# Kernel tuning notes

Hardware: AMD Instinct MI355X
Metric: run time of the kernel (lower is better)

## Reference

```python
import jax, jax.numpy as jnp
import numpy as np

N = 50000          # num nodes
E = 1_600_000      # num edges (avg degree 32)
F = 512            # node_dim
C = 64             # num_clusters
O = 256            # output_dim


def setup_inputs() -> dict:
    key = jax.random.key(0)
    ks = jax.random.split(key, 9)
    lim_p = 1.0 / np.sqrt(F)
    inp = {
        "x": jax.random.normal(ks[0], (N, F), dtype=jnp.float32),
        "edge_index": jax.random.randint(ks[1], (2, E), 0, N, dtype=jnp.int64),
        "batch": jnp.zeros((N,), dtype=jnp.int64),
        # gnn_pool: Linear(F, C)
        "Wp": jax.random.uniform(ks[2], (F, C), jnp.float32, -lim_p, lim_p),
        "bp": jax.random.uniform(ks[3], (C,), jnp.float32, -lim_p, lim_p),
        # gnn_embed: Linear(F, F)
        "We": jax.random.uniform(ks[4], (F, F), jnp.float32, -lim_p, lim_p),
        "be": jax.random.uniform(ks[5], (F,), jnp.float32, -lim_p, lim_p),
        # projection: Linear(F, O)
        "Wo": jax.random.uniform(ks[6], (F, O), jnp.float32, -lim_p, lim_p),
        "bo": jax.random.uniform(ks[7], (O,), jnp.float32, -lim_p, lim_p),
    }
    return inp


def reference(x, edge_index, batch, Wp, bp, We, be, Wo, bo):
    # s = softmax(gnn_pool(x), -1): soft cluster assignments  [N, C]
    s = jax.nn.softmax(x @ Wp + bp, axis=-1)
    # h = gnn_embed(x)  [N, F]
    h = x @ We + be
    # dense_diff_pool pooled features: out = s^T h  -> [C, F]
    # (out_adj = s^T A s and the link/entropy reg are computed by the
    #  original but discarded; they do not affect the returned output.)
    pooled = jnp.einsum("nc,nf->cf", s, h)
    # PyG dense_diff_pool unsqueezes 2D inputs to batch dim 1 -> [1, C, F]
    out = pooled[None] @ Wo + bo  # [1, C, O]
    return out
```

## Files before the change

kernel.cpp:

```cpp
#include <hip/hip_runtime.h>
#include <hip/hip_bf16.h>

typedef __attribute__((ext_vector_type(8))) short short8;
typedef __attribute__((ext_vector_type(4))) float floatx4;
typedef __attribute__((ext_vector_type(4))) unsigned uint4v;

#define FDIM 512
#define CDIM 64
#define ODIM 256
#define TR   32
#define XSF  516
#define STS 40
#define MAXP 512
#define RSW(r) ((((r) >> 3) & 3) << 2)

__device__ __forceinline__ ushort f2bf(float f) {
    union { float f; unsigned u; } v; v.f = f;
    unsigned r = v.u + 0x7FFFu + ((v.u >> 16) & 1u);
    return (ushort)(r >> 16);
}
__device__ __forceinline__ float bf2f(unsigned hi16) {
    union { unsigned u; float f; } v; v.u = hi16 << 16; return v.f;
}

__device__ __forceinline__ void gld16(const float* g, float* lds_base) {
    __builtin_amdgcn_global_load_lds(
        (const __attribute__((address_space(1))) unsigned int*)(const void*)g,
        (__attribute__((address_space(3))) unsigned int*)(void*)lds_base,
        16, 0, 0);
}

__global__ __launch_bounds__(256) void kWpT(const float* __restrict__ Wp,
                                            ushort* __restrict__ WpT) {
    int g = blockIdx.x * 256 + threadIdx.x;
    int f = g >> 6, c = g & 63;
    WpT[c * FDIM + f] = f2bf(Wp[f * CDIM + c]);
}

__global__ __launch_bounds__(512, 2) void kFused(
        const float* __restrict__ x, const ushort* __restrict__ WpT,
        const float* __restrict__ bp, ushort* __restrict__ part,
        float* __restrict__ cpart, int N, int nTiles, int P) {
    __shared__ float  xsf[TR * XSF + 16];
    __shared__ ushort sT[CDIM][STS];
    __shared__ float  red1[TR][4];
    __shared__ float  red2[TR][4];
    __shared__ float  cred[CDIM][2];

    const int t    = threadIdx.x;
    const int w    = t >> 6;
    const int lane = t & 63;
    const int l16  = lane & 15;
    const int q    = lane >> 4;
    const int ci   = w & 3;
    const int rg   = w >> 2;

    floatx4 acc[4][4];
#pragma unroll
    for (int mt = 0; mt < 4; ++mt)
#pragma unroll
        for (int nt = 0; nt < 4; ++nt) acc[mt][nt] = (floatx4){0.f, 0.f, 0.f, 0.f};
    float csp[4] = {0.f, 0.f, 0.f, 0.f};

    float bpv[4];
#pragma unroll
    for (int reg = 0; reg < 4; ++reg) bpv[reg] = bp[16 * ci + 4 * q + reg];

    const ushort* wb = WpT + (size_t)(16 * ci + l16) * FDIM + q * 8;

    for (int tile = blockIdx.x; tile < nTiles; tile += P) {
        __syncthreads();
        const int row0 = tile * TR;

#pragma unroll
        for (int i = 0; i < 8; ++i) {
            const int c0 = w * 8 + i;
            const int r  = c0 >> 1;
            const int h  = c0 & 1;
            float* lb = xsf + r * XSF + RSW(r) + h * 256;
            if (row0 + r < N) {
                const float* g = x + (size_t)(row0 + r) * FDIM + h * 256 + lane * 4;
                gld16(g, lb);
            } else {
                *(floatx4*)(lb + lane * 4) = (floatx4){0.f, 0.f, 0.f, 0.f};
            }
        }
        __syncthreads();

        floatx4 acc1 = (floatx4){0.f, 0.f, 0.f, 0.f};
        const int prow = 16 * rg + l16;
        const float* xr = xsf + prow * XSF + RSW(prow);
#pragma unroll
        for (int kb = 0; kb < 4; ++kb) {
            short8 af[4];
#pragma unroll
            for (int ki = 0; ki < 4; ++ki)
                af[ki] = *(const short8*)(wb + kb * 128 + ki * 32);
#pragma unroll
            for (int ki = 0; ki < 4; ++ki) {
                const int off = kb * 128 + ki * 32 + q * 8;
                floatx4 u0 = *(const floatx4*)(xr + off);
                floatx4 u1 = *(const floatx4*)(xr + off + 4);
                short8 b;
                b[0] = (short)f2bf(u0[0]); b[1] = (short)f2bf(u0[1]);
                b[2] = (short)f2bf(u0[2]); b[3] = (short)f2bf(u0[3]);
                b[4] = (short)f2bf(u1[0]); b[5] = (short)f2bf(u1[1]);
                b[6] = (short)f2bf(u1[2]); b[7] = (short)f2bf(u1[3]);
                acc1 = __builtin_amdgcn_mfma_f32_16x16x32_bf16(af[ki], b, acc1, 0, 0, 0);
            }
        }

        const int row = prow;
        float lg[4];
#pragma unroll
        for (int reg = 0; reg < 4; ++reg) lg[reg] = acc1[reg] + bpv[reg];
        float m = fmaxf(fmaxf(lg[0], lg[1]), fmaxf(lg[2], lg[3]));
        m = fmaxf(m, __shfl_xor(m, 16));
        m = fmaxf(m, __shfl_xor(m, 32));
        if (lane < 16) red1[16 * rg + lane][ci] = m;
        __syncthreads();
        const float rmax = fmaxf(fmaxf(red1[row][0], red1[row][1]),
                                 fmaxf(red1[row][2], red1[row][3]));
        float p = 0.f;
#pragma unroll
        for (int reg = 0; reg < 4; ++reg) {
            float e = __expf(lg[reg] - rmax);
            lg[reg] = e; p += e;
        }
        p += __shfl_xor(p, 16);
        p += __shfl_xor(p, 32);
        if (lane < 16) red2[16 * rg + lane][ci] = p;
        __syncthreads();
        const float rsi = 1.0f / (red2[row][0] + red2[row][1] +
                                  red2[row][2] + red2[row][3]);
        const bool valid = (row0 + row) < N;
#pragma unroll
        for (int reg = 0; reg < 4; ++reg) {
            float s = valid ? lg[reg] * rsi : 0.f;
            sT[16 * ci + 4 * q + reg][row] = f2bf(s);
            csp[reg] += s;
        }
        __syncthreads();

        short8 as_[4];
#pragma unroll
        for (int mt = 0; mt < 4; ++mt)
            as_[mt] = *(const short8*)&sT[16 * mt + l16][q * 8];
#pragma unroll
        for (int nt = 0; nt < 4; ++nt) {
            const int f = 64 * w + 16 * nt + l16;
            short8 b;
#pragma unroll
            for (int j = 0; j < 8; ++j)
                b[j] = (short)f2bf(xsf[(q * 8 + j) * XSF + 4 * q + f]);
#pragma unroll
            for (int mt = 0; mt < 4; ++mt)
                acc[mt][nt] = __builtin_amdgcn_mfma_f32_16x16x32_bf16(
                    as_[mt], b, acc[mt][nt], 0, 0, 0);
        }
    }

#pragma unroll
    for (int reg = 0; reg < 4; ++reg) {
        float v = csp[reg];
        v += __shfl_xor(v, 1); v += __shfl_xor(v, 2);
        v += __shfl_xor(v, 4); v += __shfl_xor(v, 8);
        if (l16 == 0) cred[16 * ci + 4 * q + reg][rg] = v;
    }
    __syncthreads();
    if (t < 64) cpart[(size_t)blockIdx.x * CDIM + t] = cred[t][0] + cred[t][1];

    ushort* xf = (ushort*)xsf;
#pragma unroll
    for (int mt = 0; mt < 4; ++mt)
#pragma unroll
        for (int nt = 0; nt < 4; ++nt)
#pragma unroll
            for (int reg = 0; reg < 4; ++reg)
                xf[(16 * mt + 4 * q + reg) * FDIM + 64 * w + 16 * nt + l16] =
                    f2bf(acc[mt][nt][reg]);
    __syncthreads();
    const uint4v* src = (const uint4v*)xf;
    uint4v* dst = (uint4v*)(part + (size_t)blockIdx.x * (CDIM * FDIM));
#pragma unroll
    for (int i = 0; i < 8; ++i)
        dst[i * 512 + t] = src[i * 512 + t];
}

__global__ __launch_bounds__(512) void kR(const ushort* __restrict__ part,
                                          const float* __restrict__ cpart,
                                          float* __restrict__ colsum,
                                          float* __restrict__ Mp,
                                          int P, int pch) {
    __shared__ float ws8[8];
    const int c = blockIdx.x, pc = blockIdx.y, t = threadIdx.x;
    const int p0 = pc * pch, p1 = min(p0 + pch, P);

    float sum = 0.f;
    const ushort* pp = part + (size_t)c * FDIM + t;
#pragma unroll 4
    for (int p = p0; p < p1; ++p)
        sum += bf2f((unsigned)pp[(size_t)p * (CDIM * FDIM)]);
    Mp[((size_t)pc * CDIM + c) * FDIM + t] = sum;

    float cv = 0.f;
    {
        int p = p0 + t;
        if (p < p1) cv = cpart[(size_t)p * CDIM + c];
    }
    cv += __shfl_xor(cv, 1);  cv += __shfl_xor(cv, 2);
    cv += __shfl_xor(cv, 4);  cv += __shfl_xor(cv, 8);
    cv += __shfl_xor(cv, 16); cv += __shfl_xor(cv, 32);
    if ((t & 63) == 0) ws8[t >> 6] = cv;
    __syncthreads();
    if (t == 0) {
        float tot = 0.f;
#pragma unroll
        for (int i = 0; i < 8; ++i) tot += ws8[i];
        atomicAdd(colsum + c, tot);
    }
}

__global__ __launch_bounds__(512) void kC(const float* __restrict__ Mp,
                                          const float* __restrict__ colsum,
                                          const float* __restrict__ We,
                                          const float* __restrict__ be,
                                          const float* __restrict__ Wo,
                                          const float* __restrict__ bo,
                                          float* __restrict__ out) {
    __shared__ float Mrow[512];
    __shared__ float pooled[512];
    __shared__ float halves[2][256];
    const int c = blockIdx.x, t = threadIdx.x;

    float sum = 0.f;
#pragma unroll
    for (int pc = 0; pc < 8; ++pc)
        sum += Mp[((size_t)pc * CDIM + c) * FDIM + t];
    Mrow[t] = sum;
    __syncthreads();

    float a = colsum[c] * be[t];
#pragma unroll 16
    for (int k = 0; k < FDIM; ++k)
        a = fmaf(Mrow[k], We[(size_t)k * FDIM + t], a);
    pooled[t] = a;
    __syncthreads();

    const int o = t & 255, h = t >> 8;
    float b = 0.f;
#pragma unroll 16
    for (int kk = 0; kk < 256; ++kk) {
        int k = h * 256 + kk;
        b = fmaf(pooled[k], Wo[(size_t)k * ODIM + o], b);
    }
    halves[h][o] = b;
    __syncthreads();
    if (t < 256)
        out[(size_t)c * ODIM + t] = halves[0][t] + halves[1][t] + bo[t];
}

extern "C" void kernel_launch(void* const* d_in, const int* in_sizes, int n_in,
                              void* d_out, int out_size, void* d_ws, size_t ws_size,
                              hipStream_t stream) {
    const float* x  = (const float*)d_in[0];
    const float* Wp = (const float*)d_in[3];
    const float* bp = (const float*)d_in[4];
    const float* We = (const float*)d_in[5];
    const float* be = (const float*)d_in[6];
    const float* Wo = (const float*)d_in[7];
    const float* bo = (const float*)d_in[8];
    float* out = (float*)d_out;

    const int N = in_sizes[0] / FDIM;
    const int nTiles = (N + TR - 1) / TR;

    char*   wsb    = (char*)d_ws;
    ushort* WpT    = (ushort*)wsb;
    float*  colsum = (float*)(wsb + 65536);
    float*  cpart  = (float*)(wsb + 66560);
    float*  Mp     = (float*)(wsb + 266752);
    const size_t PART_OFF = 1315328;
    ushort* part   = (ushort*)(wsb + PART_OFF);

    size_t avail = (ws_size > PART_OFF + 65536) ? (ws_size - PART_OFF) / 65536 : 1;
    int P = (int)(avail < (size_t)MAXP ? avail : (size_t)MAXP);
    if (P > nTiles) P = nTiles;
    if (P < 1) P = 1;
    const int pch = (P + 7) / 8;

    hipMemsetAsync(colsum, 0, 256, stream);
    kWpT<<<128, 256, 0, stream>>>(Wp, WpT);
    kFused<<<P, 512, 0, stream>>>(x, WpT, bp, part, cpart, N, nTiles, P);
    kR<<<dim3(CDIM, 8), 512, 0, stream>>>(part, cpart, colsum, Mp, P, pch);
    kC<<<CDIM, 512, 0, stream>>>(Mp, colsum, We, be, Wo, bo, out);
}
```

Baseline: 239.5 us.

## Double-buffer x tiles in fused kernel, hoist Wp fragments, vectorize partial reduction

The fused kernel now stages the next x tile into a second LDS buffer while computing on the current one, so global loads overlap the MFMA work. The Wp bf16 fragments are loaded into registers once instead of on every tile. The partial-reduction kernel reads four bf16 values per thread across four interleaved partition groups, which produces 32 partial rows that the final kernel sums. MAXP is halved to 256 to fit the doubled LDS use, and the workspace offsets are enlarged for the bigger Mp buffer. The cost is more registers and LDS per block, which may lower occupancy.

```diff
diff --git a/kernel.cpp b/kernel.cpp
--- a/kernel.cpp
+++ b/kernel.cpp
@@ -4,6 +4,7 @@
 typedef __attribute__((ext_vector_type(8))) short short8;
 typedef __attribute__((ext_vector_type(4))) float floatx4;
 typedef __attribute__((ext_vector_type(4))) unsigned uint4v;
+typedef __attribute__((ext_vector_type(4))) unsigned short ushort4v;
 
 #define FDIM 512
 #define CDIM 64
@@ -11,7 +12,7 @@
 #define TR   32
 #define XSF  516
 #define STS 40
-#define MAXP 512
+#define MAXP 256
 #define RSW(r) ((((r) >> 3) & 3) << 2)
 
 __device__ __forceinline__ ushort f2bf(float f) {
@@ -41,7 +42,7 @@
         const float* __restrict__ x, const ushort* __restrict__ WpT,
         const float* __restrict__ bp, ushort* __restrict__ part,
         float* __restrict__ cpart, int N, int nTiles, int P) {
-    __shared__ float  xsf[TR * XSF + 16];
+    __shared__ float  xsf[2][TR * XSF + 16];
     __shared__ ushort sT[CDIM][STS];
     __shared__ float  red1[TR][4];
     __shared__ float  red2[TR][4];
@@ -67,35 +68,45 @@
     for (int reg = 0; reg < 4; ++reg) bpv[reg] = bp[16 * ci + 4 * q + reg];
 
     const ushort* wb = WpT + (size_t)(16 * ci + l16) * FDIM + q * 8;
-
-    for (int tile = blockIdx.x; tile < nTiles; tile += P) {
-        __syncthreads();
-        const int row0 = tile * TR;
-
+    short8 af[4][4];
+#pragma unroll
+    for (int kb = 0; kb < 4; ++kb)
+#pragma unroll
+        for (int ki = 0; ki < 4; ++ki)
+            af[kb][ki] = *(const short8*)(wb + kb * 128 + ki * 32);
+
+    auto stage = [&](int tile, float* xb) {
+        const int row0s = tile * TR;
 #pragma unroll
         for (int i = 0; i < 8; ++i) {
             const int c0 = w * 8 + i;
             const int r  = c0 >> 1;
             const int h  = c0 & 1;
-            float* lb = xsf + r * XSF + RSW(r) + h * 256;
-            if (row0 + r < N) {
-                const float* g = x + (size_t)(row0 + r) * FDIM + h * 256 + lane * 4;
+            float* lb = xb + r * XSF + RSW(r) + h * 256;
+            if (row0s + r < N) {
+                const float* g = x + (size_t)(row0s + r) * FDIM + h * 256 + lane * 4;
                 gld16(g, lb);
             } else {
                 *(floatx4*)(lb + lane * 4) = (floatx4){0.f, 0.f, 0.f, 0.f};
             }
         }
-        __syncthreads();
+    };
+
+    stage(blockIdx.x, xsf[0]);
+    __syncthreads();
+
+    int it = 0;
+    for (int tile = blockIdx.x; tile < nTiles; tile += P, ++it) {
+        float* xb = xsf[it & 1];
+        if (tile + P < nTiles) stage(tile + P, xsf[(it & 1) ^ 1]);
+
+        const int row0 = tile * TR;
 
         floatx4 acc1 = (floatx4){0.f, 0.f, 0.f, 0.f};
         const int prow = 16 * rg + l16;
-        const float* xr = xsf + prow * XSF + RSW(prow);
+        const float* xr = xb + prow * XSF + RSW(prow);
 #pragma unroll
         for (int kb = 0; kb < 4; ++kb) {
-            short8 af[4];
-#pragma unroll
-            for (int ki = 0; ki < 4; ++ki)
-                af[ki] = *(const short8*)(wb + kb * 128 + ki * 32);
 #pragma unroll
             for (int ki = 0; ki < 4; ++ki) {
                 const int off = kb * 128 + ki * 32 + q * 8;
@@ -106,7 +117,7 @@
                 b[2] = (short)f2bf(u0[2]); b[3] = (short)f2bf(u0[3]);
                 b[4] = (short)f2bf(u1[0]); b[5] = (short)f2bf(u1[1]);
                 b[6] = (short)f2bf(u1[2]); b[7] = (short)f2bf(u1[3]);
-                acc1 = __builtin_amdgcn_mfma_f32_16x16x32_bf16(af[ki], b, acc1, 0, 0, 0);
+                acc1 = __builtin_amdgcn_mfma_f32_16x16x32_bf16(af[kb][ki], b, acc1, 0, 0, 0);
             }
         }
 
@@ -152,12 +163,14 @@
             short8 b;
 #pragma unroll
             for (int j = 0; j < 8; ++j)
-                b[j] = (short)f2bf(xsf[(q * 8 + j) * XSF + 4 * q + f]);
+                b[j] = (short)f2bf(xb[(q * 8 + j) * XSF + 4 * q + f]);
 #pragma unroll
             for (int mt = 0; mt < 4; ++mt)
                 acc[mt][nt] = __builtin_amdgcn_mfma_f32_16x16x32_bf16(
                     as_[mt], b, acc[mt][nt], 0, 0, 0);
         }
+
+        __syncthreads();
     }
 
 #pragma unroll
@@ -194,14 +207,19 @@
                                           int P, int pch) {
     __shared__ float ws8[8];
     const int c = blockIdx.x, pc = blockIdx.y, t = threadIdx.x;
+    const int g  = t >> 7;
+    const int f0 = (t & 127) << 2;
     const int p0 = pc * pch, p1 = min(p0 + pch, P);
 
-    float sum = 0.f;
-    const ushort* pp = part + (size_t)c * FDIM + t;
-#pragma unroll 4
-    for (int p = p0; p < p1; ++p)
-        sum += bf2f((unsigned)pp[(size_t)p * (CDIM * FDIM)]);
-    Mp[((size_t)pc * CDIM + c) * FDIM + t] = sum;
+    float s0 = 0.f, s1 = 0.f, s2 = 0.f, s3 = 0.f;
+    for (int p = p0 + g; p < p1; p += 4) {
+        const ushort4v v = *(const ushort4v*)(part + (size_t)p * (CDIM * FDIM)
+                                              + (size_t)c * FDIM + f0);
+        s0 += bf2f((unsigned)v[0]); s1 += bf2f((unsigned)v[1]);
+        s2 += bf2f((unsigned)v[2]); s3 += bf2f((unsigned)v[3]);
+    }
+    floatx4 o = (floatx4){s0, s1, s2, s3};
+    *(floatx4*)(Mp + (((size_t)(pc * 4 + g) * CDIM + c) * FDIM + f0)) = o;
 
     float cv = 0.f;
     {
@@ -235,7 +253,7 @@
 
     float sum = 0.f;
 #pragma unroll
-    for (int pc = 0; pc < 8; ++pc)
+    for (int pc = 0; pc < 32; ++pc)
         sum += Mp[((size_t)pc * CDIM + c) * FDIM + t];
     Mrow[t] = sum;
     __syncthreads();
@@ -280,7 +298,7 @@
     float*  colsum = (float*)(wsb + 65536);
     float*  cpart  = (float*)(wsb + 66560);
     float*  Mp     = (float*)(wsb + 266752);
-    const size_t PART_OFF = 1315328;
+    const size_t PART_OFF = 4461056;
     ushort* part   = (ushort*)(wsb + PART_OFF);
 
     size_t avail = (ws_size > PART_OFF + 65536) ? (ws_size - PART_OFF) / 65536 : 1;
```

Result: faster. 223.0 us (-6.9%).
